# Kernel tuning notes

Hardware: AMD Instinct MI355X
Metric: run time of the kernel (lower is better)

The kernel has to match this reference:

```python
import jax, jax.numpy as jnp
import numpy as np

S_LEN, T_LEN, BATCH, HID = 32, 32, 64, 512


def setup_inputs() -> dict:
    key = jax.random.key(0)
    ks = jax.random.split(key, 5)
    H = HID
    sc = lambda n: 1.0 / np.sqrt(n)
    return {
        "source": jax.random.normal(ks[0], (S_LEN, BATCH, H), jnp.float32),
        "target": jax.random.normal(ks[1], (T_LEN, BATCH, H), jnp.float32),
        # H2h Dense: concat(s_h, t_h) [B, 2H] -> [B, H], linear
        "W_H2h": (jax.random.normal(ks[2], (2 * H, H), jnp.float32) * sc(2 * H)),
        "b_H2h": jnp.zeros((H,), jnp.float32),
        # shared LSTMCell weights (Keras gate order i, f, g, o)
        "W_kernel": (jax.random.normal(ks[3], (H, 4 * H), jnp.float32) * sc(H)),
        "W_rec": (jax.random.normal(ks[4], (H, 4 * H), jnp.float32) * sc(H)),
        "b_lstm": jnp.zeros((4 * H,), jnp.float32),
    }


def _lstm_cell(x, h, c, Wk, Wr, b):
    # Keras LSTMCell math, gate order i, f, g(candidate), o
    z = x @ Wk + h @ Wr + b  # [B, 4H]
    i, f, g, o = jnp.split(z, 4, axis=-1)
    c2 = jax.nn.sigmoid(f) * c + jax.nn.sigmoid(i) * jnp.tanh(g)
    h2 = jax.nn.sigmoid(o) * jnp.tanh(c2)
    return h2, c2


def reference(source, target, W_H2h, b_H2h, W_kernel, W_rec, b_lstm):
    # source: [S, B, H] (time-major), target: [T, B, H]
    T, B, H = target.shape

    def inner(s_state, t_slice):
        # s_state carried along the target axis; t_slice is target cell j state
        s_step, s_h, s_m = s_state
        t_step, t_h, t_m = t_slice
        hmid = jnp.concatenate([s_h, t_h], axis=1) @ W_H2h + b_H2h  # [B, H]
        ns_h, ns_m = _lstm_cell(s_step, hmid, s_m, W_kernel, W_rec, b_lstm)
        nt_h, nt_m = _lstm_cell(t_step, hmid, t_m, W_kernel, W_rec, b_lstm)
        # step arrays get overwritten with the new hidden state
        return (ns_h, ns_h, ns_m), (nt_h, nt_h, nt_m)

    def outer(t_arrays, s_in):
        # fresh source state per outer step i: step = source[i], h = m = 0
        z = jnp.zeros_like(s_in)
        (s_step_f, _, _), t_new = jax.lax.scan(inner, (s_in, z, z), t_arrays)
        return t_new, s_step_f

    zeros = jnp.zeros((T, B, H), source.dtype)
    t_final, source_out = jax.lax.scan(outer, (target, zeros, zeros), source)
    return source_out, t_final[0]
```

## Files before the change

kernel.cpp:

```cpp
#include <hip/hip_runtime.h>

#define BLK 256

typedef __bf16 bf16;
typedef __bf16 bf16x8 __attribute__((ext_vector_type(8)));
typedef float f32x4 __attribute__((ext_vector_type(4)));

__device__ __forceinline__ float sigm(float x) { return 1.f / (1.f + __expf(-x)); }
__device__ __forceinline__ float tanh_(float x) {
    x = fminf(fmaxf(x, -15.f), 15.f);
    float e = __expf(2.f * x);
    return (e - 1.f) / (e + 1.f);
}

__device__ __forceinline__ void gl2lds(const bf16* g, bf16* l) {
    __builtin_amdgcn_global_load_lds((const __attribute__((address_space(1))) void*)g,
                                     (__attribute__((address_space(3))) void*)l, 16, 0, 0);
}

__global__ __launch_bounds__(256) void k_prep(
    const float* __restrict__ src, const float* __restrict__ tgt,
    const float* __restrict__ WH, const float* __restrict__ bH,
    const float* __restrict__ Wk, const float* __restrict__ Wr,
    const float* __restrict__ bl,
    bf16* __restrict__ srcb, bf16* __restrict__ tgtb,
    bf16* __restrict__ WHhi, bf16* __restrict__ WHlo,
    bf16* __restrict__ Wrhi, bf16* __restrict__ Wrlo,
    bf16* __restrict__ P2, float* __restrict__ bz) {
    __shared__ float tile[64][65];
    const int bid = blockIdx.x, t = threadIdx.x;
    if (bid < 512) {
        const float* in = (bid < 256) ? Wr : Wk;
        bf16* ohi = (bid < 256) ? Wrhi : P2;
        bf16* olo = (bid < 256) ? Wrlo : nullptr;
        const int b = bid & 255;
        const int tr = b >> 5, tc = b & 31;
#pragma unroll
        for (int q = 0; q < 16; q++) {
            int idx = q * 256 + t, lr = idx >> 6, lc = idx & 63;
            tile[lr][lc] = in[(size_t)(tr * 64 + lr) * 2048 + tc * 64 + lc];
        }
        __syncthreads();
#pragma unroll
        for (int q = 0; q < 16; q++) {
            int idx = q * 256 + t, lr = idx >> 6, lc = idx & 63;
            float v = tile[lc][lr];
            size_t o = (size_t)(tc * 64 + lr) * 512 + tr * 64 + lc;
            bf16 h = (bf16)v;
            ohi[o] = h;
            if (olo) olo[o] = (bf16)(v - (float)h);
        }
    } else if (bid < 520) {
        int c = (bid - 512) * 256 + t;
        float s = bl[c];
        for (int k = 0; k < 512; k++) s += bH[k] * Wr[(size_t)k * 2048 + c];
        bz[c] = s;
    } else {
        const int gt = (bid - 520) * 256 + t, NT = 504 * 256;
        for (int id = gt; id < 1048576; id += NT) srcb[id] = (bf16)src[id];
        for (int id = gt; id < 1048576; id += NT) tgtb[id] = (bf16)tgt[id];
        for (int id = gt; id < 524288; id += NT) {
            float v = WH[id];
            bf16 h = (bf16)v;
            WHhi[id] = h;
            WHlo[id] = (bf16)(v - (float)h);
        }
    }
}

__global__ __launch_bounds__(256, 4) void k_gemmP(
    const bf16* __restrict__ Wrhi, const bf16* __restrict__ Wrlo,
    const bf16* __restrict__ WHhi, const bf16* __restrict__ WHlo,
    const float* __restrict__ Wk,
    bf16* __restrict__ P1, bf16* __restrict__ P3,
    bf16* __restrict__ P4, bf16* __restrict__ P5) {
    __shared__ __align__(16) bf16 At[64 * 64];
    __shared__ __align__(16) bf16 Bt[128 * 64];
    const int t = threadIdx.x, w = t >> 6, l = t & 63;
    const int m0 = (blockIdx.x >> 3) * 64, n0 = (blockIdx.x & 7) * 128;
    f32x4 acc[2][4] = {};
    const bf16* Aps[3] = {Wrhi, Wrlo, Wrhi};
    const bf16* Bps[3] = {WHhi, WHhi, WHlo};
    for (int ph = 0; ph < 3; ph++) {
        const bf16* Ap = Aps[ph] + (size_t)m0 * 512;
        const bf16* Bp = Bps[ph] + (size_t)n0 * 512;
        for (int kt = 0; kt < 8; kt++) {
            int k0 = kt * 64;
            __syncthreads();
#pragma unroll
            for (int q = 0; q < 2; q++) {
                int pp = q * 256 + t;
                int r = pp >> 3, c = (pp & 7) ^ (r & 7);
                gl2lds(Ap + (size_t)r * 512 + k0 + c * 8, &At[(q * 256 + w * 64) * 8]);
            }
#pragma unroll
            for (int q = 0; q < 4; q++) {
                int pp = q * 256 + t;
                int r = pp >> 3, c = (pp & 7) ^ (r & 7);
                gl2lds(Bp + (size_t)r * 512 + k0 + c * 8, &Bt[(q * 256 + w * 64) * 8]);
            }
            __syncthreads();
#pragma unroll
            for (int ks = 0; ks < 2; ks++) {
                int c = ks * 4 + (l >> 4);
                bf16x8 af[2], bb[4];
#pragma unroll
                for (int mt = 0; mt < 2; mt++) {
                    int r = (w >> 1) * 32 + mt * 16 + (l & 15);
                    af[mt] = *(const bf16x8*)&At[(r * 8 + (c ^ (r & 7))) * 8];
                }
#pragma unroll
                for (int g = 0; g < 4; g++) {
                    int r = g * 32 + (w & 1) * 16 + (l & 15);
                    bb[g] = *(const bf16x8*)&Bt[(r * 8 + (c ^ (r & 7))) * 8];
                }
#pragma unroll
                for (int mt = 0; mt < 2; mt++)
#pragma unroll
                    for (int g = 0; g < 4; g++)
                        acc[mt][g] = __builtin_amdgcn_mfma_f32_16x16x32_bf16(
                            af[mt], bb[g], acc[mt][g], 0, 0, 0);
            }
        }
    }
    const bool hihalf = (n0 >= 512);
#pragma unroll
    for (int mt = 0; mt < 2; mt++) {
#pragma unroll
        for (int g = 0; g < 4; g++) {
            int np = n0 + g * 32 + (w & 1) * 16 + (l & 15);
#pragma unroll
            for (int r = 0; r < 4; r++) {
                int c = m0 + (w >> 1) * 32 + mt * 16 + ((l >> 4) << 2) + r;
                float v = acc[mt][g][r];
                if (!hihalf) {
                    P4[(size_t)c * 512 + np] = (bf16)v;
                    P1[(size_t)c * 512 + np] = (bf16)(v + Wk[(size_t)np * 2048 + c]);
                } else {
                    int kk = np - 512;
                    P3[(size_t)c * 512 + kk] = (bf16)v;
                    P5[(size_t)c * 512 + kk] = (bf16)(v + Wk[(size_t)kk * 2048 + c]);
                }
            }
        }
    }
}

__global__ __launch_bounds__(256, 3) void k_diag10(
    int d, int i_lo,
    const bf16* __restrict__ srcb, const bf16* __restrict__ tgtb,
    const bf16* __restrict__ P1, const bf16* __restrict__ P2,
    const bf16* __restrict__ P3, const bf16* __restrict__ P4,
    const bf16* __restrict__ P5,
    const float* __restrict__ bz,
    const bf16* __restrict__ shR, bf16* __restrict__ shW,
    const bf16* __restrict__ thR, bf16* __restrict__ thW,
    float* __restrict__ sc, float* __restrict__ tc,
    float* __restrict__ out) {
    __shared__ __align__(16) bf16 At[64 * 128];
    __shared__ __align__(16) bf16 Bt[128 * 128];
    const int t = threadIdx.x, w = t >> 6, l = t & 63;
    const int bid = blockIdx.x;
    const int xcd = bid & 7, idx = bid >> 3;
    const int p0 = idx & 1, side = (idx >> 1) & 1, cell = idx >> 2;
    const int ch0 = ((xcd << 1) | p0) << 5;
    const int i = i_lo + cell, j = d - i;
    const size_t stI = (size_t)i * 32768, stJ = (size_t)j * 32768;

    const bf16* Ah[2];
    const bf16* Wh[2];
    int nh = 0;
    if (side == 0) {
        Ah[nh] = (j == 0 ? srcb : shR) + stI;
        Wh[nh] = (j == 0 ? P2 : P1);
        nh++;
        if (i > 0) { Ah[nh] = thR + stJ; Wh[nh] = P3; nh++; }
    } else {
        if (j > 0) { Ah[nh] = shR + stI; Wh[nh] = P4; nh++; }
        Ah[nh] = (i == 0 ? tgtb : thR) + stJ;
        Wh[nh] = (i == 0 ? P2 : P5);
        nh++;
    }

    f32x4 acc[2][4] = {};
    for (int hh = 0; hh < nh; hh++) {
        const bf16* Ap = Ah[hh];
        const bf16* Wp = Wh[hh];
#pragma unroll 1
        for (int kt = 0; kt < 4; kt++) {
            int k0 = kt * 128;
            __syncthreads();
#pragma unroll
            for (int q = 0; q < 4; q++) {
                int pp = q * 256 + t;
                int r = pp >> 4, c = (pp & 15) ^ (r & 15);
                gl2lds(Ap + (size_t)r * 512 + k0 + c * 8, &At[(q * 256 + w * 64) * 8]);
            }
#pragma unroll
            for (int q = 0; q < 8; q++) {
                int pp = q * 256 + t;
                int r = pp >> 4, c = (pp & 15) ^ (r & 15);
                int g = r >> 5;
                gl2lds(Wp + (size_t)(g * 512 + ch0 + (r & 31)) * 512 + k0 + c * 8,
                       &Bt[(q * 256 + w * 64) * 8]);
            }
            __syncthreads();
#pragma unroll
            for (int ks = 0; ks < 4; ks++) {
                int cq = ks * 4 + (l >> 4);
                bf16x8 af[2], bb[4];
#pragma unroll
                for (int mt = 0; mt < 2; mt++) {
                    int r = (w >> 1) * 32 + mt * 16 + (l & 15);
                    af[mt] = *(const bf16x8*)&At[(r * 16 + (cq ^ (r & 15))) * 8];
                }
#pragma unroll
                for (int g = 0; g < 4; g++) {
                    int r = g * 32 + (w & 1) * 16 + (l & 15);
                    bb[g] = *(const bf16x8*)&Bt[(r * 16 + (cq ^ (r & 15))) * 8];
                }
#pragma unroll
                for (int mt = 0; mt < 2; mt++)
#pragma unroll
                    for (int g = 0; g < 4; g++)
                        acc[mt][g] = __builtin_amdgcn_mfma_f32_16x16x32_bf16(
                            af[mt], bb[g], acc[mt][g], 0, 0, 0);
            }
        }
    }

    const int h = ch0 + (w & 1) * 16 + (l & 15);
    float bzv[4];
#pragma unroll
    for (int g = 0; g < 4; g++) bzv[g] = bz[g * 512 + h];
#pragma unroll
    for (int mt = 0; mt < 2; mt++) {
#pragma unroll
        for (int r = 0; r < 4; r++) {
            int b = (w >> 1) * 32 + mt * 16 + ((l >> 4) << 2) + r;
            float zi = acc[mt][0][r] + bzv[0];
            float zf = acc[mt][1][r] + bzv[1];
            float zg = acc[mt][2][r] + bzv[2];
            float zo = acc[mt][3][r] + bzv[3];
            if (side == 0) {
                size_t off = stI + (size_t)b * 512 + h;
                float cold = (j == 0) ? 0.f : sc[off];
                float c2 = sigm(zf) * cold + sigm(zi) * tanh_(zg);
                float h2 = sigm(zo) * tanh_(c2);
                sc[off] = c2;
                shW[off] = (bf16)h2;
                if (j == 31) out[off] = h2;
            } else {
                size_t off = stJ + (size_t)b * 512 + h;
                float cold = (i == 0) ? 0.f : tc[off];
                float c2 = sigm(zf) * cold + sigm(zi) * tanh_(zg);
                float h2 = sigm(zo) * tanh_(c2);
                tc[off] = c2;
                thW[off] = (bf16)h2;
                if (i == 31) out[1048576 + off] = h2;
            }
        }
    }
}


extern "C" void kernel_launch(void* const* d_in, const int* in_sizes, int n_in,
                              void* d_out, int out_size, void* d_ws, size_t ws_size,
                              hipStream_t stream) {
    char* w = (char*)d_ws;
    const size_t MB = 1u << 20;
    const float* src = (const float*)d_in[0];
    const float* tgt = (const float*)d_in[1];
    const float* WH = (const float*)d_in[2];
    const float* bH = (const float*)d_in[3];
    const float* Wk = (const float*)d_in[4];
    const float* Wr = (const float*)d_in[5];
    const float* bl = (const float*)d_in[6];
    float* out = (float*)d_out;

    bf16* srcb = (bf16*)(w + 0 * MB);
    bf16* tgtb = (bf16*)(w + 2 * MB);
    bf16* WHhi = (bf16*)(w + 4 * MB);
    bf16* WHlo = (bf16*)(w + 5 * MB);
    bf16* Wrhi = (bf16*)(w + 6 * MB);
    bf16* Wrlo = (bf16*)(w + 8 * MB);
    bf16* P1 = (bf16*)(w + 10 * MB);
    bf16* P2 = (bf16*)(w + 12 * MB);
    bf16* P3 = (bf16*)(w + 14 * MB);
    bf16* P4 = (bf16*)(w + 16 * MB);
    bf16* P5 = (bf16*)(w + 18 * MB);
    float* bz = (float*)(w + 20 * MB);
    bf16* sh = (bf16*)(w + 21 * MB);
    bf16* th = (bf16*)(w + 25 * MB);
    float* sc = (float*)(w + 29 * MB);
    float* tc = (float*)(w + 33 * MB);

    k_prep<<<1024, BLK, 0, stream>>>(src, tgt, WH, bH, Wk, Wr, bl, srcb, tgtb,
                                     WHhi, WHlo, Wrhi, Wrlo, P2, bz);
    k_gemmP<<<256, BLK, 0, stream>>>(Wrhi, Wrlo, WHhi, WHlo, Wk, P1, P3, P4, P5);

    for (int d = 0; d < 63; d++) {
        int i_lo = d > 31 ? d - 31 : 0;
        int i_hi = d < 31 ? d : 31;
        int Kd = i_hi - i_lo + 1;
        const bf16* shR = sh + (size_t)(d & 1) * 1048576;
        bf16* shW = sh + (size_t)((d + 1) & 1) * 1048576;
        const bf16* thR = th + (size_t)(d & 1) * 1048576;
        bf16* thW = th + (size_t)((d + 1) & 1) * 1048576;
        k_diag10<<<Kd * 32, BLK, 0, stream>>>(d, i_lo, srcb, tgtb, P1, P2, P3, P4, P5,
                                              bz, shR, shW, thR, thW, sc, tc, out);
    }
}
```

Before: 1.391 ms.

## Double-buffer LDS tiles with async prefetch in diagonal LSTM kernel

Restructures the K loop of the wavefront kernel so LDS holds two half-width (64-column) stages. The next A/B tile is prefetched via global_load_lds while the current one feeds the MFMAs, and the loop waits with explicit vmcnt instead of a full sync before each compute. Both hidden-state contributions are flattened into one linear loop over k-chunks. The aim is to hide global load latency behind matrix math. The cost is more barriers per k, smaller tiles per iteration, and reliance on hand-counted vmcnt values being correct.

Measured after the change: 1.498 ms. 7.7% more time.

```diff
diff --git a/kernel.cpp b/kernel.cpp
--- a/kernel.cpp
+++ b/kernel.cpp
@@ -146,7 +146,7 @@
     }
 }
 
-__global__ __launch_bounds__(256, 3) void k_diag10(
+__global__ __launch_bounds__(256, 3) void k_diag11(
     int d, int i_lo,
     const bf16* __restrict__ srcb, const bf16* __restrict__ tgtb,
     const bf16* __restrict__ P1, const bf16* __restrict__ P2,
@@ -157,8 +157,8 @@
     const bf16* __restrict__ thR, bf16* __restrict__ thW,
     float* __restrict__ sc, float* __restrict__ tc,
     float* __restrict__ out) {
-    __shared__ __align__(16) bf16 At[64 * 128];
-    __shared__ __align__(16) bf16 Bt[128 * 128];
+    __shared__ __align__(16) bf16 At[2][64 * 64];
+    __shared__ __align__(16) bf16 Bt[2][128 * 64];
     const int t = threadIdx.x, w = t >> 6, l = t & 63;
     const int bid = blockIdx.x;
     const int xcd = bid & 7, idx = bid >> 3;
@@ -167,67 +167,86 @@
     const int i = i_lo + cell, j = d - i;
     const size_t stI = (size_t)i * 32768, stJ = (size_t)j * 32768;
 
-    const bf16* Ah[2];
-    const bf16* Wh[2];
-    int nh = 0;
+    const bf16 *Ah0, *Wh0, *Ah1 = nullptr, *Wh1 = nullptr;
+    int nh = 1;
     if (side == 0) {
-        Ah[nh] = (j == 0 ? srcb : shR) + stI;
-        Wh[nh] = (j == 0 ? P2 : P1);
-        nh++;
-        if (i > 0) { Ah[nh] = thR + stJ; Wh[nh] = P3; nh++; }
+        Ah0 = (j == 0 ? srcb : shR) + stI;
+        Wh0 = (j == 0 ? P2 : P1);
+        if (i > 0) { Ah1 = thR + stJ; Wh1 = P3; nh = 2; }
     } else {
-        if (j > 0) { Ah[nh] = shR + stI; Wh[nh] = P4; nh++; }
-        Ah[nh] = (i == 0 ? tgtb : thR) + stJ;
-        Wh[nh] = (i == 0 ? P2 : P5);
-        nh++;
+        if (j > 0) {
+            Ah0 = shR + stI; Wh0 = P4;
+            Ah1 = (i == 0 ? tgtb : thR) + stJ;
+            Wh1 = (i == 0 ? P2 : P5);
+            nh = 2;
+        } else {
+            Ah0 = (i == 0 ? tgtb : thR) + stJ;
+            Wh0 = (i == 0 ? P2 : P5);
+        }
     }
 
     f32x4 acc[2][4] = {};
-    for (int hh = 0; hh < nh; hh++) {
-        const bf16* Ap = Ah[hh];
-        const bf16* Wp = Wh[hh];
+    const int R = nh * 8;
+
+#define STAGE(DBF, RR)                                                          \
+    do {                                                                        \
+        const bf16* Ap_ = ((RR) < 8) ? Ah0 : Ah1;                               \
+        const bf16* Wp_ = ((RR) < 8) ? Wh0 : Wh1;                               \
+        const int k0_ = ((RR) & 7) * 64;                                        \
+        _Pragma("unroll")                                                       \
+        for (int q = 0; q < 2; q++) {                                           \
+            int pp = q * 256 + t;                                               \
+            int r = pp >> 3, c = (pp & 7) ^ (r & 7);                            \
+            gl2lds(Ap_ + (size_t)r * 512 + k0_ + c * 8,                         \
+                   &At[DBF][(q * 256 + w * 64) * 8]);                           \
+        }                                                                       \
+        _Pragma("unroll")                                                       \
+        for (int q = 0; q < 4; q++) {                                           \
+            int pp = q * 256 + t;                                               \
+            int r = pp >> 3, c = (pp & 7) ^ (r & 7);                            \
+            size_t grow = (size_t)((r >> 5) * 512 + ch0 + (r & 31));            \
+            gl2lds(Wp_ + grow * 512 + k0_ + c * 8,                              \
+                   &Bt[DBF][(q * 256 + w * 64) * 8]);                           \
+        }                                                                       \
+    } while (0)
+
+    STAGE(0, 0);
+    int bf = 0;
 #pragma unroll 1
-        for (int kt = 0; kt < 4; kt++) {
-            int k0 = kt * 128;
-            __syncthreads();
-#pragma unroll
-            for (int q = 0; q < 4; q++) {
-                int pp = q * 256 + t;
-                int r = pp >> 4, c = (pp & 15) ^ (r & 15);
-                gl2lds(Ap + (size_t)r * 512 + k0 + c * 8, &At[(q * 256 + w * 64) * 8]);
-            }
-#pragma unroll
-            for (int q = 0; q < 8; q++) {
-                int pp = q * 256 + t;
-                int r = pp >> 4, c = (pp & 15) ^ (r & 15);
-                int g = r >> 5;
-                gl2lds(Wp + (size_t)(g * 512 + ch0 + (r & 31)) * 512 + k0 + c * 8,
-                       &Bt[(q * 256 + w * 64) * 8]);
-            }
-            __syncthreads();
-#pragma unroll
-            for (int ks = 0; ks < 4; ks++) {
-                int cq = ks * 4 + (l >> 4);
-                bf16x8 af[2], bb[4];
-#pragma unroll
-                for (int mt = 0; mt < 2; mt++) {
-                    int r = (w >> 1) * 32 + mt * 16 + (l & 15);
-                    af[mt] = *(const bf16x8*)&At[(r * 16 + (cq ^ (r & 15))) * 8];
-                }
-#pragma unroll
-                for (int g = 0; g < 4; g++) {
-                    int r = g * 32 + (w & 1) * 16 + (l & 15);
-                    bb[g] = *(const bf16x8*)&Bt[(r * 16 + (cq ^ (r & 15))) * 8];
-                }
-#pragma unroll
-                for (int mt = 0; mt < 2; mt++)
-#pragma unroll
-                    for (int g = 0; g < 4; g++)
-                        acc[mt][g] = __builtin_amdgcn_mfma_f32_16x16x32_bf16(
-                            af[mt], bb[g], acc[mt][g], 0, 0, 0);
-            }
-        }
-    }
+    for (int rr = 0; rr < R; rr++) {
+        if (rr + 1 < R) {
+            STAGE(bf ^ 1, rr + 1);
+            asm volatile("s_waitcnt vmcnt(6)" ::: "memory");
+        } else {
+            asm volatile("s_waitcnt vmcnt(0)" ::: "memory");
+        }
+        __builtin_amdgcn_sched_barrier(0);
+        __builtin_amdgcn_s_barrier();
+#pragma unroll
+        for (int ks = 0; ks < 2; ks++) {
+            int cq = ks * 4 + (l >> 4);
+            bf16x8 af[2], bb[4];
+#pragma unroll
+            for (int mt = 0; mt < 2; mt++) {
+                int r = (w >> 1) * 32 + mt * 16 + (l & 15);
+                af[mt] = *(const bf16x8*)&At[bf][(r * 8 + (cq ^ (r & 7))) * 8];
+            }
+#pragma unroll
+            for (int g = 0; g < 4; g++) {
+                int r = g * 32 + (w & 1) * 16 + (l & 15);
+                bb[g] = *(const bf16x8*)&Bt[bf][(r * 8 + (cq ^ (r & 7))) * 8];
+            }
+#pragma unroll
+            for (int mt = 0; mt < 2; mt++)
+#pragma unroll
+                for (int g = 0; g < 4; g++)
+                    acc[mt][g] = __builtin_amdgcn_mfma_f32_16x16x32_bf16(
+                        af[mt], bb[g], acc[mt][g], 0, 0, 0);
+        }
+        __builtin_amdgcn_s_barrier();
+        bf ^= 1;
+    }
+#undef STAGE
 
     const int h = ch0 + (w & 1) * 16 + (l & 15);
     float bzv[4];
@@ -307,7 +326,7 @@
         bf16* shW = sh + (size_t)((d + 1) & 1) * 1048576;
         const bf16* thR = th + (size_t)(d & 1) * 1048576;
         bf16* thW = th + (size_t)((d + 1) & 1) * 1048576;
-        k_diag10<<<Kd * 32, BLK, 0, stream>>>(d, i_lo, srcb, tgtb, P1, P2, P3, P4, P5,
+        k_diag11<<<Kd * 32, BLK, 0, stream>>>(d, i_lo, srcb, tgtb, P1, P2, P3, P4, P5,
                                               bz, shR, shW, thR, thW, sc, tc, out);
     }
 }
```
